# Kernel optimization log

Hardware: AMD Instinct MI355X
Metric: run time of the kernel (lower is better)

Reference implementation:

```python
import jax, jax.numpy as jnp
import numpy as np

_DN = ('NCHW', 'OIHW', 'NCHW')

def _conv(x, w, b, stride, pad):
    y = jax.lax.conv_general_dilated(x, w, (stride, stride), [(pad, pad), (pad, pad)], dimension_numbers=_DN)
    return y + b[None, :, None, None]

def setup_inputs() -> dict:
    key = jax.random.key(0)
    ks = jax.random.split(key, 9)
    B, C, H, W = 32, 3, 128, 128
    HC, D, K = 128, 64, 512
    def he(k, shape, fan_in):
        return jax.random.normal(k, shape, jnp.float32) * np.float32(np.sqrt(2.0 / fan_in))
    return {
        'x': jax.random.normal(ks[0], (B, C, H, W), jnp.float32),
        'enc_w1': he(ks[1], (HC, C, 3, 3), C * 9),
        'enc_b1': jnp.zeros((HC,), jnp.float32),
        'enc_w2': he(ks[2], (HC, HC, 3, 3), HC * 9),
        'enc_b2': jnp.zeros((HC,), jnp.float32),
        'proj_w': he(ks[3], (D, HC, 1, 1), HC),
        'proj_b': jnp.zeros((D,), jnp.float32),
        'codebook': jax.random.uniform(ks[4], (K, D), jnp.float32, -1.0 / K, 1.0 / K),
        'dproj_w': he(ks[5], (HC, D, 1, 1), D),
        'dproj_b': jnp.zeros((HC,), jnp.float32),
        'dconv1_w': he(ks[6], (HC, HC, 3, 3), HC * 9),
        'dconv1_b': jnp.zeros((HC,), jnp.float32),
        'dconv2_w': he(ks[7], (C, HC, 1, 1), HC),
        'dconv2_b': jnp.zeros((C,), jnp.float32),
    }

def reference(x, enc_w1, enc_b1, enc_w2, enc_b2, proj_w, proj_b, codebook,
              dproj_w, dproj_b, dconv1_w, dconv1_b, dconv2_w, dconv2_b):
    beta = 0.25
    Gh = Gw = 8
    B, C, H, W = x.shape
    D = codebook.shape[1]
    sg = jax.lax.stop_gradient
    # ---- encoder ----
    h = jax.nn.relu(_conv(x, enc_w1, enc_b1, 2, 1))      # (B,HC,H/2,W/2)
    h = jax.nn.relu(_conv(h, enc_w2, enc_b2, 2, 1))      # (B,HC,H/4,W/4)
    f = h.shape[2] // Gh                                  # adaptive avg pool (exact)
    h = h.reshape(B, h.shape[1], Gh, f, Gw, f).mean(axis=(3, 5))
    z_e = _conv(h, proj_w, proj_b, 1, 0)                 # (B,D,Gh,Gw)
    # ---- vector quantizer ----
    z_flat = z_e.transpose(0, 2, 3, 1).reshape(-1, D)    # (B*Gh*Gw, D)
    dist = ((z_flat ** 2).sum(1, keepdims=True)
            + (codebook ** 2).sum(1)[None, :]
            - 2.0 * (z_flat @ codebook.T))               # (N, K)
    idx_flat = jnp.argmin(dist, axis=1)
    z_q_flat = codebook[idx_flat]                        # gather
    codebook_loss = jnp.mean((z_q_flat - sg(z_flat)) ** 2)
    commit_loss = jnp.mean((z_flat - sg(z_q_flat)) ** 2)
    vq_loss = codebook_loss + beta * commit_loss
    z_q_st = z_flat + sg(z_q_flat - z_flat)              # straight-through
    z_q = z_q_st.reshape(B, Gh, Gw, D).transpose(0, 3, 1, 2)
    idx = idx_flat.reshape(B, Gh, Gw)
    # ---- decoder ----
    y = _conv(z_q, dproj_w, dproj_b, 1, 0)               # (B,HC,Gh,Gw)
    s = H // Gh                                           # nearest upsample factor
    y = jnp.repeat(jnp.repeat(y, s, axis=2), s, axis=3)  # (B,HC,H,W)
    y = jax.nn.relu(y)
    y = jax.nn.relu(_conv(y, dconv1_w, dconv1_b, 1, 1))
    x_hat = _conv(y, dconv2_w, dconv2_b, 1, 0)           # (B,C,H,W)
    return (x_hat, idx, vq_loss, z_e)
```

## Files before the change

kernel.cpp:

```cpp
#include <hip/hip_runtime.h>
#include <math.h>


typedef _Float16 f16x8 __attribute__((ext_vector_type(8)));
typedef float f32x4 __attribute__((ext_vector_type(4)));

#define H1N 16777216
#define YTAIL (2048 * 128)

__global__ __launch_bounds__(256) void k_prep(const float* __restrict__ w2,
                                              const float* __restrict__ w1,
                                              const float* __restrict__ wp,
                                              const float* __restrict__ wd,
                                              const float* __restrict__ wd1,
                                              const float* __restrict__ cb,
                                              float* __restrict__ w1t,
                                              float* __restrict__ wpT,
                                              float* __restrict__ wdT,
                                              float* __restrict__ cbT,
                                              _Float16* __restrict__ Ah,
                                              _Float16* __restrict__ Al,
                                              _Float16* __restrict__ WS,
                                              _Float16* __restrict__ h1h) {
  int bx = blockIdx.x, tid = threadIdx.x;
  if (bx < 128) {
    __shared__ float wrow[1152];
    int co = bx;
    for (int i = tid; i < 1152; i += 256) wrow[i] = wd1[co * 1152 + i];
    __syncthreads();
    if (tid < 128) {
      int ci = tid;
      float w[9];
#pragma unroll
      for (int t = 0; t < 9; t++) w[t] = wrow[ci * 9 + t];
      float rx[3][5];
#pragma unroll
      for (int ky = 0; ky < 3; ky++) {
        float a0 = w[ky * 3 + 0], a1 = w[ky * 3 + 1], a2 = w[ky * 3 + 2];
        rx[ky][0] = a0; rx[ky][1] = a1 + a2; rx[ky][2] = a0 + a1 + a2;
        rx[ky][3] = a0 + a1; rx[ky][4] = a2;
      }
#pragma unroll
      for (int px = 0; px < 5; px++) {
        float s0 = rx[0][px], s1 = rx[1][px], s2 = rx[2][px];
        float ry[5];
        ry[0] = s0; ry[1] = s1 + s2; ry[2] = s0 + s1 + s2; ry[3] = s0 + s1; ry[4] = s2;
#pragma unroll
        for (int py = 0; py < 5; py++) {
          int pq = py * 5 + px;
          float v = ry[py];
          _Float16 h = (_Float16)v;
          int o = (pq * 128 + co) * 128 + ci;
          Ah[o] = h;
          Al[o] = (_Float16)(v - (float)h);
        }
      }
    }
    return;
  }
  if (bx < 144) {
    __shared__ float wst[9216];
    int co0 = (bx - 128) * 8;
    for (int i = tid; i < 9216; i += 256) wst[i] = w2[co0 * 1152 + i];
    __syncthreads();
    for (int i = tid; i < 9216; i += 256) {
      int co = i / 1152, r = i - co * 1152;
      int tap = r >> 7, ci = r & 127;
      float v = wst[co * 1152 + ci * 9 + tap];
      _Float16 h = (_Float16)v;
      int og = ((tap * 16 + (ci >> 3)) * 128 + co0 + co) * 8 + (ci & 7);
      WS[og] = h;
      WS[og + 147456] = (_Float16)(v - (float)h);
    }
    return;
  }
  if (bx < 152) {
    __shared__ float cbs[64 * 65];
    int k0 = (bx - 144) * 64;
    for (int i = tid; i < 4096; i += 256) {
      int k = i >> 6, d = i & 63;
      cbs[k * 65 + d] = cb[(k0 + k) * 64 + d];
    }
    __syncthreads();
    for (int i = tid; i < 4096; i += 256) {
      int d = i >> 6, k = i & 63;
      cbT[d * 512 + k0 + k] = cbs[k * 65 + d];
    }
    return;
  }
  for (int i = tid; i < 3456; i += 256) {
    int co = i & 127, t = i >> 7;
    w1t[t * 128 + co] = w1[co * 27 + t];
  }
  for (int i = tid; i < 8192; i += 256) {
    int d = i & 63, k = i >> 6;
    wpT[k * 64 + d] = wp[d * 128 + k];
  }
  for (int i = tid; i < 8192; i += 256) {
    int co = i & 127, d = i >> 7;
    wdT[d * 128 + co] = wd[co * 64 + d];
  }
  if (tid < 64) h1h[H1N + tid] = (_Float16)0.f;
}

__global__ __launch_bounds__(256) void k_conv1(const float* __restrict__ x,
                                               const float* __restrict__ w1t,
                                               const float* __restrict__ b1,
                                               _Float16* __restrict__ h1h) {
  __shared__ float E[3][9][68];
  __shared__ float O[3][9][68];
  int co_t = blockIdx.x, oh_t = blockIdx.y, b = blockIdx.z;
  int oh0 = oh_t * 4;
  int tid = threadIdx.x;
  int wv = __builtin_amdgcn_readfirstlane(tid >> 6);
  int l = tid & 63;
  int coB = co_t * 32 + wv * 8;

  for (int idx = tid; idx < 1728; idx += 256) {
    int p = idx & 63, r = idx >> 6;
    int ci = r / 9, lr = r - ci * 9;
    int ih = 2 * oh0 - 1 + lr;
    float2 v = make_float2(0.f, 0.f);
    if ((unsigned)ih < 128u)
      v = *(const float2*)&x[((b * 3 + ci) * 128 + ih) * 128 + 2 * p];
    E[ci][lr][p] = v.x;
    O[ci][lr][p + 1] = v.y;
  }
  if (tid < 27) {
    int ci = tid / 9, lr = tid - ci * 9;
    O[ci][lr][0] = 0.f;
  }
  __syncthreads();

  int ohl = l >> 4, ow0 = (l & 15) * 4;
  int oh = oh0 + ohl;
  float4 acc[8];
#pragma unroll
  for (int q = 0; q < 8; q++) {
    float bv = b1[coB + q];
    acc[q] = make_float4(bv, bv, bv, bv);
  }
#pragma unroll
  for (int ci = 0; ci < 3; ci++) {
#pragma unroll
    for (int ky = 0; ky < 3; ky++) {
      int lr = 2 * ohl + ky;
      float4 ev = *(float4*)&E[ci][lr][ow0];
      float4 od = *(float4*)&O[ci][lr][ow0];
      float o4 = O[ci][lr][ow0 + 4];
      const float* wr = w1t + (ci * 9 + ky * 3) * 128 + coB;
#pragma unroll
      for (int q = 0; q < 8; q++) {
        float wa = wr[q], wb = wr[128 + q], wc = wr[256 + q];
        acc[q].x = fmaf(wa, od.x, acc[q].x);
        acc[q].x = fmaf(wb, ev.x, acc[q].x);
        acc[q].x = fmaf(wc, od.y, acc[q].x);
        acc[q].y = fmaf(wa, od.y, acc[q].y);
        acc[q].y = fmaf(wb, ev.y, acc[q].y);
        acc[q].y = fmaf(wc, od.z, acc[q].y);
        acc[q].z = fmaf(wa, od.z, acc[q].z);
        acc[q].z = fmaf(wb, ev.z, acc[q].z);
        acc[q].z = fmaf(wc, od.w, acc[q].z);
        acc[q].w = fmaf(wa, od.w, acc[q].w);
        acc[q].w = fmaf(wb, ev.w, acc[q].w);
        acc[q].w = fmaf(wc, o4,   acc[q].w);
      }
    }
  }
  int g = coB >> 3;
  int pbase = ((g * 32 + b) * 64 + oh) * 64;
#pragma unroll
  for (int oi = 0; oi < 4; oi++) {
    f16x8 hv;
#pragma unroll
    for (int q = 0; q < 8; q++)
      hv[q] = (_Float16)fmaxf(((const float*)&acc[q])[oi], 0.f);
    *(f16x8*)&h1h[(pbase + ow0 + oi) * 8] = hv;
  }
}

#define C2_ACHUNK 4420
#define C2_WCHUNK 4680
#define C2_WOFF (C2_ACHUNK * 8)
#define C2_LDSB ((C2_ACHUNK + C2_WCHUNK) * 16)
#define C2_STEP 4194304
#define C2_WADV 4096

__global__ __launch_bounds__(512, 2) void k_conv2(const _Float16* __restrict__ h1h,
                                                  const _Float16* __restrict__ WS,
                                                  const float* __restrict__ b2,
                                                  float* __restrict__ h2) {
  extern __shared__ _Float16 L[];
  int bx = blockIdx.x;
  int cohalf = bx & 1;
  int bq = bx >> 1;
  int b = bq >> 2, ohq = bq & 3;
  int oh0 = ohq * 8;
  int tid = threadIdx.x;
  int w = tid >> 6, l = tid & 63;
  int cw = w & 1, rw = w >> 1;
  int ln = l & 15, quad = l >> 4;

  int cursA[9];
  int advA[9];
#pragma unroll
  for (int k = 0; k < 9; k++) {
    int c = (k < 8) ? (tid + k * 512) : (4096 + tid);
    if (c < C2_ACHUNK) {
      int q = c / 65, rem = c - q * 65;
      int ph = rem >= 33;
      int u = ph ? rem - 33 : rem;
      int r = q % 17, g = q / 17;
      int iw = ph ? 2 * u : 2 * u - 1;
      int ih = 2 * oh0 - 1 + r;
      bool ok = (ih >= 0) && (iw >= 0) && (iw < 64);
      cursA[k] = ok ? ((g * 32 + b) * 64 + ih) * 512 + iw * 8 : H1N;
      advA[k] = ok ? C2_STEP : 0;
    } else {
      cursA[k] = H1N;
      advA[k] = 0;
    }
  }
  int cursW[10];
#pragma unroll
  for (int k = 0; k < 10; k++) {
    int c = (k < 9) ? (tid + k * 512) : (4608 + tid);
    if (c < C2_WCHUNK) {
      int q65 = c / 65, u = c - q65 * 65;
      if (u > 63) u = 63;
      int pl = q65 >= 36;
      int r36 = q65 - pl * 36;
      int t = r36 >> 2, ci8 = r36 & 3;
      cursW[k] = ((pl * 9 + t) * 16 + ci8) * 1024 + (cohalf * 64 + u) * 8;
    } else {
      cursW[k] = 0;
    }
  }

  f32x4 acc[2][4] = {};
  for (int step = 0; step < 4; step++) {
    if (step) __syncthreads();
#pragma unroll
    for (int k = 0; k < 8; k++) {
      __builtin_amdgcn_global_load_lds(
          (const __attribute__((address_space(1))) void*)(h1h + cursA[k]),
          (__attribute__((address_space(3))) void*)&L[(tid + k * 512) * 8],
          16, 0, 0);
      cursA[k] += advA[k];
    }
    if (tid < 324)
      __builtin_amdgcn_global_load_lds(
          (const __attribute__((address_space(1))) void*)(h1h + cursA[8]),
          (__attribute__((address_space(3))) void*)&L[(4096 + tid) * 8],
          16, 0, 0);
    cursA[8] += advA[8];
#pragma unroll
    for (int k = 0; k < 9; k++) {
      __builtin_amdgcn_global_load_lds(
          (const __attribute__((address_space(1))) void*)(WS + cursW[k]),
          (__attribute__((address_space(3))) void*)&L[C2_WOFF +
                                                     (tid + k * 512) * 8],
          16, 0, 0);
      cursW[k] += C2_WADV;
    }
    if (tid < 72)
      __builtin_amdgcn_global_load_lds(
          (const __attribute__((address_space(1))) void*)(WS + cursW[9]),
          (__attribute__((address_space(3))) void*)&L[C2_WOFF +
                                                     (4608 + tid) * 8],
          16, 0, 0);
    cursW[9] += C2_WADV;
    __syncthreads();

#pragma unroll
    for (int ky = 0; ky < 3; ky++) {
#pragma unroll
      for (int kx = 0; kx < 3; kx++) {
        int t = ky * 3 + kx;
        int wb = (t * 4 + quad) * 65 + cw * 32 + ln;
        f16x8 Ah0 = *(const f16x8*)&L[C2_WOFF + wb * 8];
        f16x8 Ah1 = *(const f16x8*)&L[C2_WOFF + (wb + 16) * 8];
        f16x8 Al0 = *(const f16x8*)&L[C2_WOFF + (wb + 2340) * 8];
        f16x8 Al1 = *(const f16x8*)&L[C2_WOFF + (wb + 2356) * 8];
#pragma unroll
        for (int s = 0; s < 4; s++) {
          int owl = (s & 1) * 16 + ln;
          int r = 4 * rw + 2 * (s >> 1) + ky;
          int abase = (quad * 17 + r) * 65;
          int uoff = (kx == 1) ? (33 + owl) : (owl + (kx == 2));
          f16x8 Bh = *(const f16x8*)&L[(abase + uoff) * 8];
          acc[0][s] = __builtin_amdgcn_mfma_f32_16x16x32_f16(Al0, Bh, acc[0][s], 0, 0, 0);
          acc[0][s] = __builtin_amdgcn_mfma_f32_16x16x32_f16(Ah0, Bh, acc[0][s], 0, 0, 0);
          acc[1][s] = __builtin_amdgcn_mfma_f32_16x16x32_f16(Al1, Bh, acc[1][s], 0, 0, 0);
          acc[1][s] = __builtin_amdgcn_mfma_f32_16x16x32_f16(Ah1, Bh, acc[1][s], 0, 0, 0);
        }
      }
    }
  }
#pragma unroll
  for (int cs = 0; cs < 2; cs++)
#pragma unroll
    for (int s = 0; s < 4; s++) {
      int oh = oh0 + 2 * rw + (s >> 1);
      int ow = (s & 1) * 16 + ln;
#pragma unroll
      for (int r2 = 0; r2 < 4; r2++) {
        int co = cohalf * 64 + cw * 32 + cs * 16 + quad * 4 + r2;
        h2[((b * 128 + co) * 32 + oh) * 32 + ow] = fmaxf(acc[cs][s][r2] + b2[co], 0.f);
      }
    }
}

__global__ __launch_bounds__(256) void k_poolproj(const float* __restrict__ h2,
                                                  const float* __restrict__ wpT,
                                                  const float* __restrict__ pb,
                                                  float* __restrict__ z_e_out,
                                                  float* __restrict__ lossacc) {
  __shared__ float hp[128][16];
  __shared__ float Ws[128][64];
  int bx = blockIdx.x, tid = threadIdx.x;
  int b = bx >> 2, quarter = bx & 3;
  if (bx == 0 && tid == 0) lossacc[0] = 0.f;
  for (int i = tid; i < 8192; i += 256) Ws[i >> 6][i & 63] = wpT[i];
  for (int i = tid; i < 2048; i += 256) {
    int ci = i >> 4, pl = i & 15;
    int pi = quarter * 16 + pl;
    int bi = pi >> 3, bj = pi & 7;
    const float* src = &h2[((b * 128 + ci) * 32 + bi * 4) * 32 + bj * 4];
    float4 r0 = *(const float4*)src;
    float4 r1 = *(const float4*)(src + 32);
    float4 r2 = *(const float4*)(src + 64);
    float4 r3 = *(const float4*)(src + 96);
    float s = r0.x + r0.y + r0.z + r0.w + r1.x + r1.y + r1.z + r1.w +
              r2.x + r2.y + r2.z + r2.w + r3.x + r3.y + r3.z + r3.w;
    hp[ci][pl] = s * 0.0625f;
  }
  __syncthreads();
  int d = tid >> 2, s0 = (tid & 3) * 4;
  float4 acc = make_float4(0.f, 0.f, 0.f, 0.f);
  for (int k = 0; k < 128; k++) {
    float a = Ws[k][d];
    float4 h = *(float4*)&hp[k][s0];
    acc.x = fmaf(a, h.x, acc.x);
    acc.y = fmaf(a, h.y, acc.y);
    acc.z = fmaf(a, h.z, acc.z);
    acc.w = fmaf(a, h.w, acc.w);
  }
  float bv = pb[d];
  float4 r4 = make_float4(acc.x + bv, acc.y + bv, acc.z + bv, acc.w + bv);
  *(float4*)&z_e_out[(b * 64 + d) * 64 + quarter * 16 + s0] = r4;
}

__global__ __launch_bounds__(256) void k_vqdproj(const float* __restrict__ z_e,
                                                 const float* __restrict__ cbT,
                                                 const float* __restrict__ cb,
                                                 const float* __restrict__ wdT,
                                                 const float* __restrict__ db,
                                                 float* __restrict__ idx_f,
                                                 _Float16* __restrict__ Yh,
                                                 _Float16* __restrict__ Yl,
                                                 float* __restrict__ loss_acc) {
  __shared__ float zs[64];
  __shared__ float zqv[64];
  __shared__ double wbst[4];
  __shared__ int wbi[4];
  int n = blockIdx.x, tid = threadIdx.x;
  int b = n >> 6, pi = n & 63;
  if (tid < 64) zs[tid] = z_e[(b * 64 + tid) * 64 + pi];
  if (n == 0 && tid < 64) {
    Yh[YTAIL + tid] = (_Float16)0.f;
    Yh[YTAIL + 64 + tid] = (_Float16)0.f;
    Yl[YTAIL + tid] = (_Float16)0.f;
    Yl[YTAIL + 64 + tid] = (_Float16)0.f;
  }
  __syncthreads();
  int w = tid >> 6, lane = tid & 63;
  double best = 1e300;
  int bi = 0;
#pragma unroll
  for (int j = 0; j < 2; j++) {
    int k = w * 128 + j * 64 + lane;
    double a0 = 0.0, a1 = 0.0, a2 = 0.0, a3 = 0.0;
#pragma unroll 4
    for (int d = 0; d < 64; d += 4) {
      double f0 = (double)zs[d] - (double)cbT[d * 512 + k];
      double f1 = (double)zs[d + 1] - (double)cbT[(d + 1) * 512 + k];
      double f2 = (double)zs[d + 2] - (double)cbT[(d + 2) * 512 + k];
      double f3 = (double)zs[d + 3] - (double)cbT[(d + 3) * 512 + k];
      a0 = fma(f0, f0, a0);
      a1 = fma(f1, f1, a1);
      a2 = fma(f2, f2, a2);
      a3 = fma(f3, f3, a3);
    }
    double acc = (a0 + a1) + (a2 + a3);
    if (acc < best) { best = acc; bi = k; }
  }
  for (int m = 1; m < 64; m <<= 1) {
    double ob = __shfl_xor(best, m, 64);
    int oi = __shfl_xor(bi, m, 64);
    if (ob < best || (ob == best && oi < bi)) { best = ob; bi = oi; }
  }
  if (lane == 0) { wbst[w] = best; wbi[w] = bi; }
  __syncthreads();
  best = wbst[0];
  bi = wbi[0];
#pragma unroll
  for (int q = 1; q < 4; q++) {
    double ob = wbst[q];
    int oi = wbi[q];
    if (ob < best || (ob == best && oi < bi)) { best = ob; bi = oi; }
  }
  if (tid < 64) {
    float zq_l = cb[bi * 64 + tid];
    float e = zq_l - zs[tid];
    float sq = e * e;
    for (int m = 1; m < 64; m <<= 1) sq += __shfl_xor(sq, m, 64);
    if (tid == 0) {
      idx_f[n] = (float)bi;
      atomicAdd(loss_acc, sq);
    }
    zqv[tid] = zq_l;
  }
  __syncthreads();
  if (tid < 128) {
    float a = db[tid];
#pragma unroll 4
    for (int d = 0; d < 64; d++) a = fmaf(wdT[d * 128 + tid], zqv[d], a);
    float y = fmaxf(a, 0.f);
    _Float16 h = (_Float16)y;
    Yh[n * 128 + tid] = h;
    Yl[n * 128 + tid] = (_Float16)(y - (float)h);
  }
}

__global__ __launch_bounds__(256) void k_dec(const _Float16* __restrict__ Yh,
                                             const _Float16* __restrict__ Yl,
                                             const _Float16* __restrict__ Ah,
                                             const _Float16* __restrict__ Al,
                                             float* __restrict__ G) {
  int bxx = blockIdx.x;
  int pq = bxx >> 6, n_t = bxx & 63;
  int w = threadIdx.x >> 6, l = threadIdx.x & 63;
  int ln = l & 15, quad = l >> 4;
  int coW = w * 32;
  int nB = n_t * 32;
  int py = pq / 5, px = pq - py * 5;
  int dy = (py == 0) ? -1 : ((py == 4) ? 1 : 0);
  int dx = (px == 0) ? -1 : ((px == 4) ? 1 : 0);
  int src[2];
#pragma unroll
  for (int s = 0; s < 2; s++) {
    int n = nB + s * 16 + ln;
    int bb = n >> 6, s6 = n & 63;
    int sy = (s6 >> 3) + dy, sx = (s6 & 7) + dx;
    bool ok = ((unsigned)sy < 8u) && ((unsigned)sx < 8u);
    src[s] = ok ? ((bb * 64 + sy * 8 + sx) * 128) : YTAIL;
  }
  int kq = quad * 8;
  f32x4 acc[2][2] = {};
#pragma unroll 2
  for (int ci0 = 0; ci0 < 128; ci0 += 32) {
    const int wbase = (pq * 128 + coW + ln) * 128 + ci0 + kq;
    f16x8 Ah0 = *(const f16x8*)&Ah[wbase];
    f16x8 Al0 = *(const f16x8*)&Al[wbase];
    f16x8 Ah1 = *(const f16x8*)&Ah[wbase + 2048];
    f16x8 Al1 = *(const f16x8*)&Al[wbase + 2048];
    f16x8 Bh[2], Bl[2];
#pragma unroll
    for (int s = 0; s < 2; s++) {
      Bh[s] = *(const f16x8*)&Yh[src[s] + ci0 + kq];
      Bl[s] = *(const f16x8*)&Yl[src[s] + ci0 + kq];
    }
#pragma unroll
    for (int cs = 0; cs < 2; cs++) {
      f16x8 ah = cs ? Ah1 : Ah0;
      f16x8 al = cs ? Al1 : Al0;
#pragma unroll
      for (int s = 0; s < 2; s++) {
        acc[cs][s] = __builtin_amdgcn_mfma_f32_16x16x32_f16(al, Bh[s], acc[cs][s], 0, 0, 0);
        acc[cs][s] = __builtin_amdgcn_mfma_f32_16x16x32_f16(ah, Bl[s], acc[cs][s], 0, 0, 0);
        acc[cs][s] = __builtin_amdgcn_mfma_f32_16x16x32_f16(ah, Bh[s], acc[cs][s], 0, 0, 0);
      }
    }
  }
#pragma unroll
  for (int cs = 0; cs < 2; cs++)
#pragma unroll
    for (int s = 0; s < 2; s++) {
      int site = nB + s * 16 + ln;
      float4 g = make_float4(acc[cs][s][0], acc[cs][s][1], acc[cs][s][2], acc[cs][s][3]);
      *(float4*)&G[(pq * 2048 + site) * 128 + coW + cs * 16 + quad * 4] = g;
    }
}

__global__ __launch_bounds__(256) void k_out(const float* __restrict__ G,
                                             const float* __restrict__ bc1,
                                             const float* __restrict__ w3,
                                             const float* __restrict__ b3,
                                             float* __restrict__ xhat,
                                             const float* __restrict__ loss_acc,
                                             float* __restrict__ out_loss) {
  __shared__ float Tb[9][128];
  __shared__ float part[9][3][8];
  __shared__ float vals[9][3];
  int bj = blockIdx.x, bi = blockIdx.y, b = blockIdx.z;
  int s = bi * 8 + bj;
  int n = b * 64 + s;
  int tid = threadIdx.x;
  if (bj == 0 && bi == 0 && b == 0 && tid == 0)
    out_loss[0] = loss_acc[0] * 1.25f / 131072.0f;
  int co = tid & 127, h = tid >> 7;
  const int rset[3][2] = {{0, 1}, {2, 2}, {3, 4}};
  const int rcnt[3] = {2, 1, 2};
  for (int cls = h; cls < 9; cls += 2) {
    int r = cls / 3, c = cls - r * 3;
    float sum = bc1[co];
    for (int iy = 0; iy < rcnt[r]; iy++) {
      int py = rset[r][iy];
      for (int ix = 0; ix < rcnt[c]; ix++) {
        int px = rset[c][ix];
        sum += G[((py * 5 + px) * 2048 + n) * 128 + co];
      }
    }
    Tb[cls][co] = fmaxf(sum, 0.f);
  }
  __syncthreads();
  if (tid < 216) {
    int cls = tid / 24, rem = tid - cls * 24;
    int cc = rem >> 3, seg = rem & 7;
    float ss = 0.f;
#pragma unroll
    for (int d = 0; d < 16; d++) ss = fmaf(w3[cc * 128 + seg * 16 + d], Tb[cls][seg * 16 + d], ss);
    part[cls][cc][seg] = ss;
  }
  __syncthreads();
  if (tid < 27) {
    int cls = tid / 3, cc = tid - cls * 3;
    float ss = b3[cc];
#pragma unroll
    for (int seg = 0; seg < 8; seg++) ss += part[cls][cc][seg];
    vals[cls][cc] = ss;
  }
  __syncthreads();
  for (int i = tid; i < 768; i += 256) {
    int cc = i >> 8, p = i & 255;
    int ry = p >> 4, rx = p & 15;
    int rcls = (ry == 0) ? 0 : ((ry == 15) ? 2 : 1);
    int ccls = (rx == 0) ? 0 : ((rx == 15) ? 2 : 1);
    xhat[((b * 3 + cc) * 128 + bi * 16 + ry) * 128 + bj * 16 + rx] =
        vals[rcls * 3 + ccls][cc];
  }
}

extern "C" void kernel_launch(void* const* d_in, const int* in_sizes, int n_in,
                              void* d_out, int out_size, void* d_ws, size_t ws_size,
                              hipStream_t stream) {
  const float* x   = (const float*)d_in[0];
  const float* w1  = (const float*)d_in[1];
  const float* b1  = (const float*)d_in[2];
  const float* w2  = (const float*)d_in[3];
  const float* b2  = (const float*)d_in[4];
  const float* wp  = (const float*)d_in[5];
  const float* pb  = (const float*)d_in[6];
  const float* cb  = (const float*)d_in[7];
  const float* wd  = (const float*)d_in[8];
  const float* db  = (const float*)d_in[9];
  const float* wc1 = (const float*)d_in[10];
  const float* bc1 = (const float*)d_in[11];
  const float* wc2 = (const float*)d_in[12];
  const float* bc2 = (const float*)d_in[13];
  float* out = (float*)d_out;
  float* ws  = (float*)d_ws;

  _Float16* h1h = (_Float16*)(ws);
  float* h2     = ws + 16777280;
  _Float16* WS  = (_Float16*)(ws + 20971584);
  float* w1t    = ws + 21119040;
  float* wpT    = ws + 21122496;
  float* wdT    = ws + 21130688;
  float* cbT    = ws + 21138880;
  _Float16* Ahd = (_Float16*)(ws + 21171648);
  _Float16* Ald = (_Float16*)(ws + 21376448);
  float* G       = ws;
  _Float16* Yh   = (_Float16*)(ws + 6553600);
  _Float16* Yl   = (_Float16*)(ws + 6684736);
  float* lossacc = ws + 6815872;

  float* o_xhat = out;
  float* o_idx  = out + 1572864;
  float* o_loss = out + 1574912;
  float* o_ze   = out + 1574913;

  static bool s_attr_done = false;
  if (!s_attr_done) {
    (void)hipFuncSetAttribute((const void*)k_conv2,
                              hipFuncAttributeMaxDynamicSharedMemorySize, C2_LDSB);
    s_attr_done = true;
  }

  k_prep<<<dim3(153), 256, 0, stream>>>(w2, w1, wp, wd, wc1, cb,
                                        w1t, wpT, wdT, cbT, Ahd, Ald, WS, h1h);
  k_conv1<<<dim3(4, 16, 32), 256, 0, stream>>>(x, w1t, b1, h1h);
  k_conv2<<<dim3(256), 512, C2_LDSB, stream>>>(h1h, WS, b2, h2);
  k_poolproj<<<dim3(128), 256, 0, stream>>>(h2, wpT, pb, o_ze, lossacc);
  k_vqdproj<<<dim3(2048), 256, 0, stream>>>(o_ze, cbT, cb, wdT, db, o_idx, Yh, Yl, lossacc);
  k_dec<<<dim3(1600), 256, 0, stream>>>(Yh, Yl, Ahd, Ald, G);
  k_out<<<dim3(8, 8, 32), 256, 0, stream>>>(G, bc1, wc2, bc2, o_xhat, lossacc, o_loss);
}
```

Baseline: 237.0 us.

## Accumulate per-class tap sums inside k_dec and fuse bias+ReLU there

k_dec now computes, for each of the 9 boundary classes, the sum over its 1-4 per-position weight variants directly in MFMA accumulators, and applies bias and ReLU before storing. This replaces 25 partial G outputs with 9 final T buffers, cutting global writes and k_out's reduction reads. The grid shrinks from 1600 to 576 blocks, each doing variable work (1-4 passes), which may cause load imbalance and lower parallelism.

```diff
diff --git a/kernel.cpp b/kernel.cpp
--- a/kernel.cpp
+++ b/kernel.cpp
@@ -437,49 +437,59 @@
                                              const _Float16* __restrict__ Yl,
                                              const _Float16* __restrict__ Ah,
                                              const _Float16* __restrict__ Al,
-                                             float* __restrict__ G) {
+                                             const float* __restrict__ bc1,
+                                             float* __restrict__ Tb) {
   int bxx = blockIdx.x;
-  int pq = bxx >> 6, n_t = bxx & 63;
+  int cls = bxx >> 6, n_t = bxx & 63;
+  int rc = cls / 3, c3 = cls - rc * 3;
+  const int rset[3][2] = {{0, 1}, {2, 2}, {3, 4}};
+  const int rcnt[3] = {2, 1, 2};
   int w = threadIdx.x >> 6, l = threadIdx.x & 63;
   int ln = l & 15, quad = l >> 4;
   int coW = w * 32;
   int nB = n_t * 32;
-  int py = pq / 5, px = pq - py * 5;
-  int dy = (py == 0) ? -1 : ((py == 4) ? 1 : 0);
-  int dx = (px == 0) ? -1 : ((px == 4) ? 1 : 0);
-  int src[2];
-#pragma unroll
-  for (int s = 0; s < 2; s++) {
-    int n = nB + s * 16 + ln;
-    int bb = n >> 6, s6 = n & 63;
-    int sy = (s6 >> 3) + dy, sx = (s6 & 7) + dx;
-    bool ok = ((unsigned)sy < 8u) && ((unsigned)sx < 8u);
-    src[s] = ok ? ((bb * 64 + sy * 8 + sx) * 128) : YTAIL;
-  }
   int kq = quad * 8;
   f32x4 acc[2][2] = {};
+  for (int iy = 0; iy < rcnt[rc]; iy++) {
+    int py = rset[rc][iy];
+    int dy = (py == 0) ? -1 : ((py == 4) ? 1 : 0);
+    for (int ix = 0; ix < rcnt[c3]; ix++) {
+      int px = rset[c3][ix];
+      int dx = (px == 0) ? -1 : ((px == 4) ? 1 : 0);
+      int pq = py * 5 + px;
+      int src[2];
+#pragma unroll
+      for (int s = 0; s < 2; s++) {
+        int n = nB + s * 16 + ln;
+        int bb = n >> 6, s6 = n & 63;
+        int sy = (s6 >> 3) + dy, sx = (s6 & 7) + dx;
+        bool ok = ((unsigned)sy < 8u) && ((unsigned)sx < 8u);
+        src[s] = ok ? ((bb * 64 + sy * 8 + sx) * 128) : YTAIL;
+      }
 #pragma unroll 2
-  for (int ci0 = 0; ci0 < 128; ci0 += 32) {
-    const int wbase = (pq * 128 + coW + ln) * 128 + ci0 + kq;
-    f16x8 Ah0 = *(const f16x8*)&Ah[wbase];
-    f16x8 Al0 = *(const f16x8*)&Al[wbase];
-    f16x8 Ah1 = *(const f16x8*)&Ah[wbase + 2048];
-    f16x8 Al1 = *(const f16x8*)&Al[wbase + 2048];
-    f16x8 Bh[2], Bl[2];
-#pragma unroll
-    for (int s = 0; s < 2; s++) {
-      Bh[s] = *(const f16x8*)&Yh[src[s] + ci0 + kq];
-      Bl[s] = *(const f16x8*)&Yl[src[s] + ci0 + kq];
-    }
-#pragma unroll
-    for (int cs = 0; cs < 2; cs++) {
-      f16x8 ah = cs ? Ah1 : Ah0;
-      f16x8 al = cs ? Al1 : Al0;
-#pragma unroll
-      for (int s = 0; s < 2; s++) {
-        acc[cs][s] = __builtin_amdgcn_mfma_f32_16x16x32_f16(al, Bh[s], acc[cs][s], 0, 0, 0);
-        acc[cs][s] = __builtin_amdgcn_mfma_f32_16x16x32_f16(ah, Bl[s], acc[cs][s], 0, 0, 0);
-        acc[cs][s] = __builtin_amdgcn_mfma_f32_16x16x32_f16(ah, Bh[s], acc[cs][s], 0, 0, 0);
+      for (int ci0 = 0; ci0 < 128; ci0 += 32) {
+        const int wbase = (pq * 128 + coW + ln) * 128 + ci0 + kq;
+        f16x8 Ah0 = *(const f16x8*)&Ah[wbase];
+        f16x8 Al0 = *(const f16x8*)&Al[wbase];
+        f16x8 Ah1 = *(const f16x8*)&Ah[wbase + 2048];
+        f16x8 Al1 = *(const f16x8*)&Al[wbase + 2048];
+        f16x8 Bh[2], Bl[2];
+#pragma unroll
+        for (int s = 0; s < 2; s++) {
+          Bh[s] = *(const f16x8*)&Yh[src[s] + ci0 + kq];
+          Bl[s] = *(const f16x8*)&Yl[src[s] + ci0 + kq];
+        }
+#pragma unroll
+        for (int cs = 0; cs < 2; cs++) {
+          f16x8 ah = cs ? Ah1 : Ah0;
+          f16x8 al = cs ? Al1 : Al0;
+#pragma unroll
+          for (int s = 0; s < 2; s++) {
+            acc[cs][s] = __builtin_amdgcn_mfma_f32_16x16x32_f16(al, Bh[s], acc[cs][s], 0, 0, 0);
+            acc[cs][s] = __builtin_amdgcn_mfma_f32_16x16x32_f16(ah, Bl[s], acc[cs][s], 0, 0, 0);
+            acc[cs][s] = __builtin_amdgcn_mfma_f32_16x16x32_f16(ah, Bh[s], acc[cs][s], 0, 0, 0);
+          }
+        }
       }
     }
   }
@@ -488,13 +498,17 @@
 #pragma unroll
     for (int s = 0; s < 2; s++) {
       int site = nB + s * 16 + ln;
-      float4 g = make_float4(acc[cs][s][0], acc[cs][s][1], acc[cs][s][2], acc[cs][s][3]);
-      *(float4*)&G[(pq * 2048 + site) * 128 + coW + cs * 16 + quad * 4] = g;
-    }
-}
-
-__global__ __launch_bounds__(256) void k_out(const float* __restrict__ G,
-                                             const float* __restrict__ bc1,
+      int co0 = coW + cs * 16 + quad * 4;
+      float4 bv = *(const float4*)&bc1[co0];
+      float4 g = make_float4(fmaxf(acc[cs][s][0] + bv.x, 0.f),
+                             fmaxf(acc[cs][s][1] + bv.y, 0.f),
+                             fmaxf(acc[cs][s][2] + bv.z, 0.f),
+                             fmaxf(acc[cs][s][3] + bv.w, 0.f));
+      *(float4*)&Tb[(cls * 2048 + site) * 128 + co0] = g;
+    }
+}
+
+__global__ __launch_bounds__(256) void k_out(const float* __restrict__ TbG,
                                              const float* __restrict__ w3,
                                              const float* __restrict__ b3,
                                              float* __restrict__ xhat,
@@ -509,20 +523,9 @@
   int tid = threadIdx.x;
   if (bj == 0 && bi == 0 && b == 0 && tid == 0)
     out_loss[0] = loss_acc[0] * 1.25f / 131072.0f;
-  int co = tid & 127, h = tid >> 7;
-  const int rset[3][2] = {{0, 1}, {2, 2}, {3, 4}};
-  const int rcnt[3] = {2, 1, 2};
-  for (int cls = h; cls < 9; cls += 2) {
-    int r = cls / 3, c = cls - r * 3;
-    float sum = bc1[co];
-    for (int iy = 0; iy < rcnt[r]; iy++) {
-      int py = rset[r][iy];
-      for (int ix = 0; ix < rcnt[c]; ix++) {
-        int px = rset[c][ix];
-        sum += G[((py * 5 + px) * 2048 + n) * 128 + co];
-      }
-    }
-    Tb[cls][co] = fmaxf(sum, 0.f);
+  for (int i = tid; i < 1152; i += 256) {
+    int cls = i >> 7, co = i & 127;
+    Tb[cls][co] = TbG[(cls * 2048 + n) * 128 + co];
   }
   __syncthreads();
   if (tid < 216) {
@@ -581,7 +584,7 @@
   float* cbT    = ws + 21138880;
   _Float16* Ahd = (_Float16*)(ws + 21171648);
   _Float16* Ald = (_Float16*)(ws + 21376448);
-  float* G       = ws;
+  float* Tb      = ws;
   _Float16* Yh   = (_Float16*)(ws + 6553600);
   _Float16* Yl   = (_Float16*)(ws + 6684736);
   float* lossacc = ws + 6815872;
@@ -604,6 +607,6 @@
   k_conv2<<<dim3(256), 512, C2_LDSB, stream>>>(h1h, WS, b2, h2);
   k_poolproj<<<dim3(128), 256, 0, stream>>>(h2, wpT, pb, o_ze, lossacc);
   k_vqdproj<<<dim3(2048), 256, 0, stream>>>(o_ze, cbT, cb, wdT, db, o_idx, Yh, Yl, lossacc);
-  k_dec<<<dim3(1600), 256, 0, stream>>>(Yh, Yl, Ahd, Ald, G);
-  k_out<<<dim3(8, 8, 32), 256, 0, stream>>>(G, bc1, wc2, bc2, o_xhat, lossacc, o_loss);
-}
+  k_dec<<<dim3(576), 256, 0, stream>>>(Yh, Yl, Ahd, Ald, bc1, Tb);
+  k_out<<<dim3(8, 8, 32), 256, 0, stream>>>(Tb, wc2, bc2, o_xhat, lossacc, o_loss);
+}
```

Measured after the change: 228.6 us. 1.04x faster.
